# Kernel tuning notes

Measured on AMD Instinct MI355X. Metric: run time of the kernel, lower is better.

## Reference

```python
import jax, jax.numpy as jnp
import numpy as np
from jax.ops import segment_sum

N_NODES = 100000


def gcn_norm(edge_index, edge_weight, num_nodes):
    # Add self-loops with weight 1 (PyG gcn_norm default fill_value=1.0)
    loop = jnp.arange(num_nodes, dtype=edge_index.dtype)
    src = jnp.concatenate([edge_index[0], loop])
    dst = jnp.concatenate([edge_index[1], loop])
    w = jnp.concatenate([edge_weight, jnp.ones((num_nodes,), edge_weight.dtype)])
    deg = segment_sum(w, dst, num_segments=num_nodes)  # in-degree (col)
    dis = jnp.where(deg > 0, jax.lax.rsqrt(deg), 0.0)
    norm = dis[src] * w * dis[dst]
    return src, dst, norm


def gcn_conv(x, src, dst, norm, W, b, num_nodes):
    xw = x @ W                       # [N, out] linear first (small out dim)
    msg = xw[src] * norm[:, None]    # gather + scale, [E+N, out]
    out = segment_sum(msg, dst, num_segments=num_nodes)
    return out + b


def setup_inputs() -> dict:
    key = jax.random.key(0)
    ks = jax.random.split(key, 6)
    N, E, Cin, H, Cout = N_NODES, 3200000, 512, 16, 40
    x = jax.random.normal(ks[0], (N, Cin), dtype=jnp.float32)
    edge_index = jax.random.randint(ks[1], (2, E), 0, N, dtype=jnp.int64)
    edge_weight = jax.random.uniform(ks[2], (E,), dtype=jnp.float32)
    W1 = jax.random.normal(ks[3], (Cin, H), dtype=jnp.float32) / np.sqrt(Cin)
    b1 = jnp.zeros((H,), jnp.float32)
    W2 = jax.random.normal(ks[4], (H, Cout), dtype=jnp.float32) / np.sqrt(H)
    b2 = jnp.zeros((Cout,), jnp.float32)
    return {"x": x, "edge_index": edge_index, "edge_weight": edge_weight,
            "W1": W1, "b1": b1, "W2": W2, "b2": b2}


def reference(x, edge_index, edge_weight, W1, b1, W2, b2):
    N = x.shape[0]
    # gcn_norm computed once; GCNConv(cached=True) reuses it for both layers
    src, dst, norm = gcn_norm(edge_index, edge_weight, N)
    h = jax.nn.relu(gcn_conv(x, src, dst, norm, W1, b1, N))
    # F.dropout(training=self.training): identity in eval mode
    h = gcn_conv(h, src, dst, norm, W2, b2, N)
    return jax.nn.log_softmax(h, axis=1)
```

## Files before the change

### kernel.cpp

```cpp
#include <hip/hip_runtime.h>

#define CIN  512
#define HDIM 16
#define CODIM 40
#define BINSZ 256
#define BSHIFT 8
#define NBMAX 512
#define EB 4096
#define CAP 9216
#define CSR_CH 9
#define WSTR 36

__device__ __forceinline__ void fma4(float4& a, float s, float4 b) {
  a.x = fmaf(s, b.x, a.x);
  a.y = fmaf(s, b.y, a.y);
  a.z = fmaf(s, b.z, a.z);
  a.w = fmaf(s, b.w, a.w);
}

__device__ __forceinline__ float4 red4(float4 v) {
  v.x += __shfl_xor(v.x, 1); v.y += __shfl_xor(v.y, 1);
  v.z += __shfl_xor(v.z, 1); v.w += __shfl_xor(v.w, 1);
  v.x += __shfl_xor(v.x, 2); v.y += __shfl_xor(v.y, 2);
  v.z += __shfl_xor(v.z, 2); v.w += __shfl_xor(v.w, 2);
  return v;
}

__device__ __forceinline__ float4 shx4(float4 v, int m) {
  return make_float4(__shfl_xor(v.x, m), __shfl_xor(v.y, m),
                     __shfl_xor(v.z, m), __shfl_xor(v.w, m));
}

__device__ __forceinline__ float4 bf4(ushort4 u) {
  return make_float4(__uint_as_float((unsigned)u.x << 16),
                     __uint_as_float((unsigned)u.y << 16),
                     __uint_as_float((unsigned)u.z << 16),
                     __uint_as_float((unsigned)u.w << 16));
}
__device__ __forceinline__ unsigned short f2bf(float f) {
  unsigned u = __float_as_uint(f);
  return (unsigned short)((u + 0x7FFFu + ((u >> 16) & 1u)) >> 16);
}
__device__ __forceinline__ ushort4 pk4(float4 v) {
  ushort4 r;
  r.x = f2bf(v.x); r.y = f2bf(v.y); r.z = f2bf(v.z); r.w = f2bf(v.w);
  return r;
}
__device__ __forceinline__ unsigned pk2(float lo, float hi) {
  return (unsigned)f2bf(lo) | ((unsigned)f2bf(hi) << 16);
}
__device__ __forceinline__ float bl(unsigned u) { return __uint_as_float(u << 16); }
__device__ __forceinline__ float bh(unsigned u) { return __uint_as_float(u & 0xFFFF0000u); }

__global__ void k_zero(int* __restrict__ p, int n) {
  int i = blockIdx.x * 256 + threadIdx.x;
  if (i < n) p[i] = 0;
}

__global__ __launch_bounds__(256) void k_binB(const int* __restrict__ src,
                                              const int* __restrict__ dst,
                                              const float* __restrict__ w,
                                              int* __restrict__ cursor,
                                              uint2* __restrict__ binned, int E) {
  __shared__ int hist[NBMAX];
  __shared__ int base[NBMAX];
  int t = threadIdx.x;
  for (int i = t; i < NBMAX; i += 256) hist[i] = 0;
  __syncthreads();
  int beg = blockIdx.x * EB, end = min(E, beg + EB);
  int dbuf[EB / 256];
  #pragma unroll
  for (int j = 0; j < EB / 256; ++j) {
    int e = beg + t + j * 256;
    int d = (e < end) ? dst[e] : -1;
    dbuf[j] = d;
    if (d >= 0) atomicAdd(&hist[d >> BSHIFT], 1);
  }
  __syncthreads();
  for (int i = t; i < NBMAX; i += 256) {
    int h = hist[i];
    base[i] = h ? (i * CAP + atomicAdd(&cursor[i], h)) : 0;
  }
  __syncthreads();
  #pragma unroll
  for (int j = 0; j < EB / 256; ++j) {
    int e = beg + t + j * 256;
    int d = dbuf[j];
    if (d >= 0) {
      int b = d >> BSHIFT;
      int pos = atomicAdd(&base[b], 1);
      binned[pos] = make_uint2((unsigned)src[e] | ((unsigned)(d & (BINSZ - 1)) << 17),
                               __float_as_uint(w[e]));
    }
  }
}

__global__ __launch_bounds__(256) void k_scanBins(
    const int* __restrict__ cnt, int* __restrict__ binoff,
    int* __restrict__ rowptr, int NB, int N) {
  __shared__ int ts[256];
  int t = threadIdx.x;
  int c0 = (2 * t     < NB) ? cnt[2 * t]     : 0;
  int c1 = (2 * t + 1 < NB) ? cnt[2 * t + 1] : 0;
  int s = c0 + c1;
  ts[t] = s;
  __syncthreads();
  #pragma unroll
  for (int off = 1; off < 256; off <<= 1) {
    int v = (t >= off) ? ts[t - off] : 0;
    __syncthreads();
    ts[t] += v;
    __syncthreads();
  }
  int ex = ts[t] - s;
  if (2 * t     < NB) binoff[2 * t]     = ex;
  if (2 * t + 1 < NB) binoff[2 * t + 1] = ex + c0;
  if (t == 255) { binoff[NB] = ts[255]; rowptr[N] = ts[255]; }
}

__global__ __launch_bounds__(1024) void k_csrbin(
    const int* __restrict__ binoff, const uint2* __restrict__ binned,
    int* __restrict__ rowptr, int2* __restrict__ csr,
    float* __restrict__ dis, int N) {
  __shared__ int   hist[BINSZ];
  __shared__ int   loff[BINSZ];
  __shared__ int   rank[BINSZ];
  __shared__ float dsum[BINSZ];
  int t = threadIdx.x, b = blockIdx.x;
  if (t < BINSZ) { hist[t] = 0; rank[t] = 0; dsum[t] = 1.0f; }
  __syncthreads();
  int cbeg = binoff[b], cnt = binoff[b + 1] - cbeg;
  size_t pbeg = (size_t)b * CAP;
  uint2 ebuf[CSR_CH];
  #pragma unroll
  for (int j = 0; j < CSR_CH; ++j) {
    int i = t + j * 1024;
    uint2 e = (i < cnt) ? binned[pbeg + i] : make_uint2(0u, 0u);
    ebuf[j] = e;
    if (i < cnt) {
      int dl = e.x >> 17;
      atomicAdd(&hist[dl], 1);
      atomicAdd(&dsum[dl], __uint_as_float(e.y));
    }
  }
  __syncthreads();
  if (t < BINSZ) loff[t] = hist[t];
  __syncthreads();
  #pragma unroll
  for (int off = 1; off < BINSZ; off <<= 1) {
    int v = 0;
    if (t < BINSZ && t >= off) v = loff[t - off];
    __syncthreads();
    if (t < BINSZ) loff[t] += v;
    __syncthreads();
  }
  if (t < BINSZ) {
    int ex = loff[t] - hist[t];
    int n = b * BINSZ + t;
    if (n < N) {
      rowptr[n] = cbeg + ex;
      dis[n] = rsqrtf(dsum[t]);
    }
    loff[t] = ex;
  }
  __syncthreads();
  #pragma unroll
  for (int j = 0; j < CSR_CH; ++j) {
    int i = t + j * 1024;
    if (i < cnt) {
      uint2 e = ebuf[j];
      int dl = e.x >> 17;
      int r = atomicAdd(&rank[dl], 1);
      csr[cbeg + loff[dl] + r] = make_int2((int)(e.x & 0x1FFFFu), (int)e.y);
    }
  }
}

__device__ __forceinline__ void dot16(float4& a0, float4& a1, float4& a2, float4& a3,
                                      uint4 U0, uint4 U1, float s) {
  a0.x = fmaf(s, bl(U0.x), a0.x); a0.y = fmaf(s, bh(U0.x), a0.y);
  a0.z = fmaf(s, bl(U0.y), a0.z); a0.w = fmaf(s, bh(U0.y), a0.w);
  a1.x = fmaf(s, bl(U0.z), a1.x); a1.y = fmaf(s, bh(U0.z), a1.y);
  a1.z = fmaf(s, bl(U0.w), a1.z); a1.w = fmaf(s, bh(U0.w), a1.w);
  a2.x = fmaf(s, bl(U1.x), a2.x); a2.y = fmaf(s, bh(U1.x), a2.y);
  a2.z = fmaf(s, bl(U1.y), a2.z); a2.w = fmaf(s, bh(U1.y), a2.w);
  a3.x = fmaf(s, bl(U1.z), a3.x); a3.y = fmaf(s, bh(U1.z), a3.y);
  a3.z = fmaf(s, bl(U1.w), a3.z); a3.w = fmaf(s, bh(U1.w), a3.w);
}

__global__ __launch_bounds__(256, 4) void k_gemm1(
    const float* __restrict__ x, const float* __restrict__ W1,
    const float* __restrict__ dis, unsigned short* __restrict__ y1, int N) {
  __shared__ unsigned w1s[128 * WSTR];
  int t = threadIdx.x;
  const float4* W14 = (const float4*)W1;
  for (int lin = t; lin < 2048; lin += 256) {
    float4 v = W14[lin];
    int g = lin >> 4, f = lin & 15;
    unsigned* p = w1s + g * WSTR + (f >> 2) * 8 + (f & 3) * 2;
    p[0] = pk2(v.x, v.y);
    p[1] = pk2(v.z, v.w);
  }
  __syncthreads();

  int quad = t >> 2;
  int q = t & 3;
  int n = blockIdx.x * 64 + quad;
  if (n >= N) return;

  const float4* xr = (const float4*)x + (size_t)n * (CIN / 4);
  float4 a0 = make_float4(0.f, 0.f, 0.f, 0.f), a1 = a0, a2 = a0, a3 = a0;

  #pragma unroll 4
  for (int kk = 0; kk < 32; ++kk) {
    float4 xa = xr[kk * 4 + q];
    const uint4* wr = (const uint4*)(w1s + (kk * 4 + q) * WSTR);
    dot16(a0, a1, a2, a3, wr[0], wr[1], xa.x);
    dot16(a0, a1, a2, a3, wr[2], wr[3], xa.y);
    dot16(a0, a1, a2, a3, wr[4], wr[5], xa.z);
    dot16(a0, a1, a2, a3, wr[6], wr[7], xa.w);
  }
  a0 = red4(a0); a1 = red4(a1); a2 = red4(a2); a3 = red4(a3);

  float d = dis[n];
  float4 sel = (q == 0) ? a0 : (q == 1) ? a1 : (q == 2) ? a2 : a3;
  sel.x *= d; sel.y *= d; sel.z *= d; sel.w *= d;
  ((ushort4*)y1)[(size_t)n * 4 + q] = pk4(sel);
}

__device__ __forceinline__ float4 rowAccB(const int2* __restrict__ csr,
                                          const ushort4* __restrict__ v4,
                                          float4 s0, int beg, int end, int q) {
  float4 s1 = make_float4(0.f, 0.f, 0.f, 0.f), s2 = s1, s3 = s1;
  int i = beg;
  for (; i + 3 < end; i += 4) {
    int2 e0 = csr[i], e1 = csr[i + 1], e2 = csr[i + 2], e3 = csr[i + 3];
    ushort4 u0 = v4[(size_t)e0.x * 4 + q];
    ushort4 u1 = v4[(size_t)e1.x * 4 + q];
    ushort4 u2 = v4[(size_t)e2.x * 4 + q];
    ushort4 u3 = v4[(size_t)e3.x * 4 + q];
    fma4(s0, __int_as_float(e0.y), bf4(u0));
    fma4(s1, __int_as_float(e1.y), bf4(u1));
    fma4(s2, __int_as_float(e2.y), bf4(u2));
    fma4(s3, __int_as_float(e3.y), bf4(u3));
  }
  for (; i < end; ++i) {
    int2 e = csr[i];
    fma4(s0, __int_as_float(e.y), bf4(v4[(size_t)e.x * 4 + q]));
  }
  s0.x += s1.x + s2.x + s3.x;
  s0.y += s1.y + s2.y + s3.y;
  s0.z += s1.z + s2.z + s3.z;
  s0.w += s1.w + s2.w + s3.w;
  return s0;
}

__global__ __launch_bounds__(256) void k_aggZ(
    const int* __restrict__ rowptr, const int2* __restrict__ csr,
    const unsigned short* __restrict__ vals, unsigned short* __restrict__ zb,
    const float* __restrict__ dis, const float* __restrict__ b1, int N) {
  int t = threadIdx.x;
  int node = blockIdx.x * 64 + (t >> 2);
  int q = t & 3;
  if (node >= N) return;
  const ushort4* v4 = (const ushort4*)vals;
  float4 a = rowAccB(csr, v4, bf4(v4[(size_t)node * 4 + q]),
                     rowptr[node], rowptr[node + 1], q);
  float d = dis[node];
  float4 bb = ((const float4*)b1)[q];
  float4 z;
  z.x = d * fmaxf(fmaf(d, a.x, bb.x), 0.f);
  z.y = d * fmaxf(fmaf(d, a.y, bb.y), 0.f);
  z.z = d * fmaxf(fmaf(d, a.z, bb.z), 0.f);
  z.w = d * fmaxf(fmaf(d, a.w, bb.w), 0.f);
  ((ushort4*)zb)[(size_t)node * 4 + q] = pk4(z);
}

__global__ __launch_bounds__(256) void k_aggF(
    const int* __restrict__ rowptr, const int2* __restrict__ csr,
    const unsigned short* __restrict__ vals, float* __restrict__ out,
    const float* __restrict__ dis, const float* __restrict__ W2,
    const float* __restrict__ b2, int N) {
  __shared__ float w2s[HDIM * CODIM + CODIM];
  int t = threadIdx.x;
  for (int i = t; i < HDIM * CODIM; i += 256) w2s[i] = W2[i];
  if (t < CODIM) w2s[HDIM * CODIM + t] = b2[t];
  __syncthreads();

  int node = blockIdx.x * 64 + (t >> 2);
  int q = t & 3;
  if (node >= N) return;
  const ushort4* v4 = (const ushort4*)vals;
  float4 a = rowAccB(csr, v4, bf4(v4[(size_t)node * 4 + q]),
                     rowptr[node], rowptr[node + 1], q);
  float d = dis[node];
  a.x *= d; a.y *= d; a.z *= d; a.w *= d;

  float4 f1 = shx4(a, 1), f2 = shx4(a, 2), f3 = shx4(a, 3);

  int col0 = q * 10;
  float v[10];
  #pragma unroll
  for (int jj = 0; jj < 10; ++jj) v[jj] = w2s[HDIM * CODIM + col0 + jj];

  {
    const float* wr;
    wr = w2s + ((q ^ 0) * 4 + 0) * CODIM + col0;
    #pragma unroll
    for (int jj = 0; jj < 10; ++jj) v[jj] = fmaf(a.x, wr[jj], v[jj]);
    wr = w2s + ((q ^ 0) * 4 + 1) * CODIM + col0;
    #pragma unroll
    for (int jj = 0; jj < 10; ++jj) v[jj] = fmaf(a.y, wr[jj], v[jj]);
    wr = w2s + ((q ^ 0) * 4 + 2) * CODIM + col0;
    #pragma unroll
    for (int jj = 0; jj < 10; ++jj) v[jj] = fmaf(a.z, wr[jj], v[jj]);
    wr = w2s + ((q ^ 0) * 4 + 3) * CODIM + col0;
    #pragma unroll
    for (int jj = 0; jj < 10; ++jj) v[jj] = fmaf(a.w, wr[jj], v[jj]);

    wr = w2s + ((q ^ 1) * 4 + 0) * CODIM + col0;
    #pragma unroll
    for (int jj = 0; jj < 10; ++jj) v[jj] = fmaf(f1.x, wr[jj], v[jj]);
    wr = w2s + ((q ^ 1) * 4 + 1) * CODIM + col0;
    #pragma unroll
    for (int jj = 0; jj < 10; ++jj) v[jj] = fmaf(f1.y, wr[jj], v[jj]);
    wr = w2s + ((q ^ 1) * 4 + 2) * CODIM + col0;
    #pragma unroll
    for (int jj = 0; jj < 10; ++jj) v[jj] = fmaf(f1.z, wr[jj], v[jj]);
    wr = w2s + ((q ^ 1) * 4 + 3) * CODIM + col0;
    #pragma unroll
    for (int jj = 0; jj < 10; ++jj) v[jj] = fmaf(f1.w, wr[jj], v[jj]);

    wr = w2s + ((q ^ 2) * 4 + 0) * CODIM + col0;
    #pragma unroll
    for (int jj = 0; jj < 10; ++jj) v[jj] = fmaf(f2.x, wr[jj], v[jj]);
    wr = w2s + ((q ^ 2) * 4 + 1) * CODIM + col0;
    #pragma unroll
    for (int jj = 0; jj < 10; ++jj) v[jj] = fmaf(f2.y, wr[jj], v[jj]);
    wr = w2s + ((q ^ 2) * 4 + 2) * CODIM + col0;
    #pragma unroll
    for (int jj = 0; jj < 10; ++jj) v[jj] = fmaf(f2.z, wr[jj], v[jj]);
    wr = w2s + ((q ^ 2) * 4 + 3) * CODIM + col0;
    #pragma unroll
    for (int jj = 0; jj < 10; ++jj) v[jj] = fmaf(f2.w, wr[jj], v[jj]);

    wr = w2s + ((q ^ 3) * 4 + 0) * CODIM + col0;
    #pragma unroll
    for (int jj = 0; jj < 10; ++jj) v[jj] = fmaf(f3.x, wr[jj], v[jj]);
    wr = w2s + ((q ^ 3) * 4 + 1) * CODIM + col0;
    #pragma unroll
    for (int jj = 0; jj < 10; ++jj) v[jj] = fmaf(f3.y, wr[jj], v[jj]);
    wr = w2s + ((q ^ 3) * 4 + 2) * CODIM + col0;
    #pragma unroll
    for (int jj = 0; jj < 10; ++jj) v[jj] = fmaf(f3.z, wr[jj], v[jj]);
    wr = w2s + ((q ^ 3) * 4 + 3) * CODIM + col0;
    #pragma unroll
    for (int jj = 0; jj < 10; ++jj) v[jj] = fmaf(f3.w, wr[jj], v[jj]);
  }

  float m = v[0];
  #pragma unroll
  for (int jj = 1; jj < 10; ++jj) m = fmaxf(m, v[jj]);
  m = fmaxf(m, __shfl_xor(m, 1));
  m = fmaxf(m, __shfl_xor(m, 2));
  float sum = 0.f;
  #pragma unroll
  for (int jj = 0; jj < 10; ++jj) sum += __expf(v[jj] - m);
  sum += __shfl_xor(sum, 1);
  sum += __shfl_xor(sum, 2);
  float lse = __logf(sum) + m;
  float* o = out + (size_t)node * CODIM + col0;
  #pragma unroll
  for (int jj = 0; jj < 10; ++jj) o[jj] = v[jj] - lse;
}

extern "C" void kernel_launch(void* const* d_in, const int* in_sizes, int n_in,
                              void* d_out, int out_size, void* d_ws, size_t ws_size,
                              hipStream_t stream) {
  const float* x  = (const float*)d_in[0];
  const int*   ei = (const int*)d_in[1];
  const float* ew = (const float*)d_in[2];
  const float* W1 = (const float*)d_in[3];
  const float* b1 = (const float*)d_in[4];
  const float* W2 = (const float*)d_in[5];
  const float* b2 = (const float*)d_in[6];
  float* out = (float*)d_out;

  int N = in_sizes[0] / CIN;
  int E = in_sizes[2];
  const int* src = ei;
  const int* dst = ei + E;
  int NB = (N + BINSZ - 1) >> BSHIFT;

  size_t NA = ((size_t)N + 255) & ~(size_t)255;
  size_t NP = ((size_t)N + 2) & ~(size_t)1;
  int*   cursor = (int*)d_ws;
  int*   binoff = cursor + NBMAX;
  int*   rowptr = binoff + NBMAX + 4;
  int2*  csr    = (int2*)(rowptr + NP);
  float* dis    = (float*)(csr + E);
  unsigned short* zb = (unsigned short*)(dis + NA);
  uint2* binned = (uint2*)(zb + NA * 16);
  unsigned short* y1 = (unsigned short*)binned;

  int gG   = (N + 63) / 64;
  int gEB  = (E + EB - 1) / EB;

  k_zero    <<<(NB + 255) / 256, 256, 0, stream>>>(cursor, NB);
  k_binB    <<<gEB, 256, 0, stream>>>(src, dst, ew, cursor, binned, E);
  k_scanBins<<<1, 256, 0, stream>>>(cursor, binoff, rowptr, NB, N);
  k_csrbin  <<<NB, 1024, 0, stream>>>(binoff, binned, rowptr, csr, dis, N);

  k_gemm1   <<<gG, 256, 0, stream>>>(x, W1, dis, y1, N);
  k_aggZ    <<<gG, 256, 0, stream>>>(rowptr, csr, y1, zb, dis, b1, N);
  k_aggF    <<<gG, 256, 0, stream>>>(rowptr, csr, zb, out, dis, W2, b2, N);
}
```

Before: 267.5 us.

## Vectorize binning loads, use wave-shuffle scan, and unroll CSR gather by eight

The binning kernel now has each thread load four contiguous dst/src/weight entries as int4/float4 instead of strided scalars. The CSR-build kernel reads pairs of binned entries as uint4 and replaces the shared-memory Hillis-Steele scan with a wave-shuffle scan plus per-wave offsets. The aggregation row loop is unrolled to eight edges to keep more gathers in flight. These aim to cut memory instruction count and barrier overhead, at the cost of more registers and reliance on 16-byte alignment of the arrays and of odd bin offsets.

```diff
diff --git a/kernel.cpp b/kernel.cpp
--- a/kernel.cpp
+++ b/kernel.cpp
@@ -8,7 +8,6 @@
 #define NBMAX 512
 #define EB 4096
 #define CAP 9216
-#define CSR_CH 9
 #define WSTR 36
 
 __device__ __forceinline__ void fma4(float4& a, float s, float4 b) {
@@ -68,13 +67,27 @@
   for (int i = t; i < NBMAX; i += 256) hist[i] = 0;
   __syncthreads();
   int beg = blockIdx.x * EB, end = min(E, beg + EB);
-  int dbuf[EB / 256];
-  #pragma unroll
-  for (int j = 0; j < EB / 256; ++j) {
-    int e = beg + t + j * 256;
-    int d = (e < end) ? dst[e] : -1;
-    dbuf[j] = d;
-    if (d >= 0) atomicAdd(&hist[d >> BSHIFT], 1);
+  int dbuf[16];
+  #pragma unroll
+  for (int j = 0; j < 4; ++j) {
+    int e = beg + t * 4 + j * 1024;
+    if (e + 3 < end) {
+      int4 d4 = *(const int4*)(dst + e);
+      dbuf[4 * j + 0] = d4.x; dbuf[4 * j + 1] = d4.y;
+      dbuf[4 * j + 2] = d4.z; dbuf[4 * j + 3] = d4.w;
+      atomicAdd(&hist[d4.x >> BSHIFT], 1);
+      atomicAdd(&hist[d4.y >> BSHIFT], 1);
+      atomicAdd(&hist[d4.z >> BSHIFT], 1);
+      atomicAdd(&hist[d4.w >> BSHIFT], 1);
+    } else {
+      #pragma unroll
+      for (int k = 0; k < 4; ++k) {
+        int ee = e + k;
+        int d = (ee < end) ? dst[ee] : -1;
+        dbuf[4 * j + k] = d;
+        if (d >= 0) atomicAdd(&hist[d >> BSHIFT], 1);
+      }
+    }
   }
   __syncthreads();
   for (int i = t; i < NBMAX; i += 256) {
@@ -83,14 +96,33 @@
   }
   __syncthreads();
   #pragma unroll
-  for (int j = 0; j < EB / 256; ++j) {
-    int e = beg + t + j * 256;
-    int d = dbuf[j];
-    if (d >= 0) {
-      int b = d >> BSHIFT;
-      int pos = atomicAdd(&base[b], 1);
-      binned[pos] = make_uint2((unsigned)src[e] | ((unsigned)(d & (BINSZ - 1)) << 17),
-                               __float_as_uint(w[e]));
+  for (int j = 0; j < 4; ++j) {
+    int e = beg + t * 4 + j * 1024;
+    if (e + 3 < end) {
+      int4   s4 = *(const int4*)(src + e);
+      float4 w4 = *(const float4*)(w + e);
+      int ss[4] = {s4.x, s4.y, s4.z, s4.w};
+      float ww[4] = {w4.x, w4.y, w4.z, w4.w};
+      #pragma unroll
+      for (int k = 0; k < 4; ++k) {
+        int d = dbuf[4 * j + k];
+        int b = d >> BSHIFT;
+        int pos = atomicAdd(&base[b], 1);
+        binned[pos] = make_uint2((unsigned)ss[k] | ((unsigned)(d & (BINSZ - 1)) << 17),
+                                 __float_as_uint(ww[k]));
+      }
+    } else {
+      #pragma unroll
+      for (int k = 0; k < 4; ++k) {
+        int ee = e + k;
+        int d = dbuf[4 * j + k];
+        if (d >= 0) {
+          int b = d >> BSHIFT;
+          int pos = atomicAdd(&base[b], 1);
+          binned[pos] = make_uint2((unsigned)src[ee] | ((unsigned)(d & (BINSZ - 1)) << 17),
+                                   __float_as_uint(w[ee]));
+        }
+      }
     }
   }
 }
@@ -126,36 +158,52 @@
   __shared__ int   loff[BINSZ];
   __shared__ int   rank[BINSZ];
   __shared__ float dsum[BINSZ];
+  __shared__ int   wsum[4];
   int t = threadIdx.x, b = blockIdx.x;
   if (t < BINSZ) { hist[t] = 0; rank[t] = 0; dsum[t] = 1.0f; }
   __syncthreads();
   int cbeg = binoff[b], cnt = binoff[b + 1] - cbeg;
   size_t pbeg = (size_t)b * CAP;
-  uint2 ebuf[CSR_CH];
-  #pragma unroll
-  for (int j = 0; j < CSR_CH; ++j) {
-    int i = t + j * 1024;
-    uint2 e = (i < cnt) ? binned[pbeg + i] : make_uint2(0u, 0u);
-    ebuf[j] = e;
-    if (i < cnt) {
+  uint4 eb2[5];
+  #pragma unroll
+  for (int j = 0; j < 5; ++j) {
+    int p = t + j * 1024;
+    int i0 = p * 2;
+    if (i0 + 1 < cnt) {
+      uint4 E2 = *(const uint4*)(binned + pbeg + i0);
+      eb2[j] = E2;
+      int dl0 = E2.x >> 17, dl1 = E2.z >> 17;
+      atomicAdd(&hist[dl0], 1);
+      atomicAdd(&dsum[dl0], __uint_as_float(E2.y));
+      atomicAdd(&hist[dl1], 1);
+      atomicAdd(&dsum[dl1], __uint_as_float(E2.w));
+    } else if (i0 < cnt) {
+      uint2 e = binned[pbeg + i0];
+      eb2[j].x = e.x; eb2[j].y = e.y;
       int dl = e.x >> 17;
       atomicAdd(&hist[dl], 1);
       atomicAdd(&dsum[dl], __uint_as_float(e.y));
     }
   }
   __syncthreads();
-  if (t < BINSZ) loff[t] = hist[t];
-  __syncthreads();
-  #pragma unroll
-  for (int off = 1; off < BINSZ; off <<= 1) {
-    int v = 0;
-    if (t < BINSZ && t >= off) v = loff[t - off];
-    __syncthreads();
-    if (t < BINSZ) loff[t] += v;
-    __syncthreads();
-  }
+  int h = 0, inc = 0;
   if (t < BINSZ) {
-    int ex = loff[t] - hist[t];
+    h = hist[t];
+    inc = h;
+    #pragma unroll
+    for (int off = 1; off < 64; off <<= 1) {
+      int v = __shfl_up(inc, off);
+      if ((t & 63) >= off) inc += v;
+    }
+    if ((t & 63) == 63) wsum[t >> 6] = inc;
+  }
+  __syncthreads();
+  if (t < BINSZ) {
+    int wid = t >> 6;
+    int wadd = 0;
+    #pragma unroll
+    for (int wv = 0; wv < 3; ++wv) if (wv < wid) wadd += wsum[wv];
+    int ex = inc - h + wadd;
     int n = b * BINSZ + t;
     if (n < N) {
       rowptr[n] = cbeg + ex;
@@ -165,13 +213,20 @@
   }
   __syncthreads();
   #pragma unroll
-  for (int j = 0; j < CSR_CH; ++j) {
-    int i = t + j * 1024;
-    if (i < cnt) {
-      uint2 e = ebuf[j];
-      int dl = e.x >> 17;
+  for (int j = 0; j < 5; ++j) {
+    int p = t + j * 1024;
+    int i0 = p * 2;
+    if (i0 < cnt) {
+      unsigned ex = eb2[j].x, ey = eb2[j].y;
+      int dl = ex >> 17;
       int r = atomicAdd(&rank[dl], 1);
-      csr[cbeg + loff[dl] + r] = make_int2((int)(e.x & 0x1FFFFu), (int)e.y);
+      csr[cbeg + loff[dl] + r] = make_int2((int)(ex & 0x1FFFFu), (int)ey);
+    }
+    if (i0 + 1 < cnt) {
+      unsigned ez = eb2[j].z, ew = eb2[j].w;
+      int dl = ez >> 17;
+      int r = atomicAdd(&rank[dl], 1);
+      csr[cbeg + loff[dl] + r] = make_int2((int)(ez & 0x1FFFFu), (int)ew);
     }
   }
 }
@@ -233,16 +288,25 @@
                                           float4 s0, int beg, int end, int q) {
   float4 s1 = make_float4(0.f, 0.f, 0.f, 0.f), s2 = s1, s3 = s1;
   int i = beg;
-  for (; i + 3 < end; i += 4) {
-    int2 e0 = csr[i], e1 = csr[i + 1], e2 = csr[i + 2], e3 = csr[i + 3];
+  for (; i + 7 < end; i += 8) {
+    int2 e0 = csr[i],     e1 = csr[i + 1], e2 = csr[i + 2], e3 = csr[i + 3];
+    int2 e4 = csr[i + 4], e5 = csr[i + 5], e6 = csr[i + 6], e7 = csr[i + 7];
     ushort4 u0 = v4[(size_t)e0.x * 4 + q];
     ushort4 u1 = v4[(size_t)e1.x * 4 + q];
     ushort4 u2 = v4[(size_t)e2.x * 4 + q];
     ushort4 u3 = v4[(size_t)e3.x * 4 + q];
+    ushort4 u4 = v4[(size_t)e4.x * 4 + q];
+    ushort4 u5 = v4[(size_t)e5.x * 4 + q];
+    ushort4 u6 = v4[(size_t)e6.x * 4 + q];
+    ushort4 u7 = v4[(size_t)e7.x * 4 + q];
     fma4(s0, __int_as_float(e0.y), bf4(u0));
     fma4(s1, __int_as_float(e1.y), bf4(u1));
     fma4(s2, __int_as_float(e2.y), bf4(u2));
     fma4(s3, __int_as_float(e3.y), bf4(u3));
+    fma4(s0, __int_as_float(e4.y), bf4(u4));
+    fma4(s1, __int_as_float(e5.y), bf4(u5));
+    fma4(s2, __int_as_float(e6.y), bf4(u6));
+    fma4(s3, __int_as_float(e7.y), bf4(u7));
   }
   for (; i < end; ++i) {
     int2 e = csr[i];
```

New measurement: 249.0 us (median of 2 runs). 1.07x faster.
